# Kernel optimization log

Hardware: AMD Instinct MI355X
Metric: run time of the kernel (lower is better)

The kernel has to match this reference:

```python
import jax, jax.numpy as jnp
import numpy as np

VOL_RANGE = (-40.0, -40.0, -1.0, 40.0, 40.0, 5.4)
VOXEL = 0.8
SCENE = tuple(int((VOL_RANGE[i + 3] - VOL_RANGE[i]) / VOXEL) for i in range(3))  # (100, 100, 8)
B, G, F = 1, 128, 16


def _make_grid():
    # generate_grid(scene_shape, offset=0.5) * voxel_size + vol_range[:3]
    axes = [(jnp.arange(s, dtype=jnp.float32) + 0.5) * VOXEL + VOL_RANGE[i]
            for i, s in enumerate(SCENE)]
    gx, gy, gz = jnp.meshgrid(*axes, indexing='ij')
    return jnp.stack([gx, gy, gz], axis=-1).reshape(-1, 3)  # (N, 3)


def setup_inputs() -> dict:
    key = jax.random.key(0)
    k1, k2, k3, k4 = jax.random.split(key, 4)
    lo = jnp.array(VOL_RANGE[:3], dtype=jnp.float32)
    hi = jnp.array(VOL_RANGE[3:], dtype=jnp.float32)
    means3d = lo + jax.random.uniform(k1, (B, G, 3), dtype=jnp.float32) * (hi - lo)
    opacities = jax.random.uniform(k2, (B, G, 1), dtype=jnp.float32)
    features = jax.random.normal(k3, (B, G, F), dtype=jnp.float32)
    A = jax.random.normal(k4, (B, G, 3, 3), dtype=jnp.float32)
    covariances = jnp.einsum('bgij,bgkj->bgik', A, A) + 0.1 * jnp.eye(3, dtype=jnp.float32)
    return {
        'grid_coords': _make_grid(),
        'means3d': means3d,
        'opacities': opacities,
        'features': features,
        'covariances': covariances,
    }


def _splat_into_3d(grid_coords, means3d, opacities, covariances, features):
    # grid_coords: (N,3); means3d: (B,G,3); opacities: (B,G,1);
    # covariances: (B,G,3,3); features: (B,G,F)
    b, g, _ = means3d.shape
    n = grid_coords.shape[0]
    f = features.shape[-1]
    dtype = means3d.dtype

    def step(carry, xs):
        dens, feats, cnts = carry                 # (B,N,1), (B,N,F), (B,N,1)
        mean, opac, cov, feat = xs                # (B,3), (B,1), (B,3,3), (B,F)
        diff = grid_coords[None] - mean[:, None]  # (B,N,3)
        cov_inv = jnp.linalg.inv(cov)             # (B,3,3)
        maha = jnp.einsum('bni,bij,bnj->bn', diff, cov_inv, diff)[..., None]  # (B,N,1)
        mask = (maha <= 4.0).astype(dtype)        # (B,N,1)
        cnts = cnts + mask
        denom = jnp.maximum(cnts, 1e-6)
        w = jnp.exp(-0.5 * maha)                  # (B,N,1)
        d_g = opac[:, None] * w                   # (B,N,1)
        dens = dens + mask * (d_g - dens) / denom
        f_g = (opac * feat)[:, None] * w          # (B,N,F)
        feats = feats + mask * (f_g - feats) / denom
        return (dens, feats, cnts), None

    init = (jnp.zeros((b, n, 1), dtype),
            jnp.zeros((b, n, f), dtype),
            jnp.zeros((b, n, 1), dtype))
    xs = (jnp.swapaxes(means3d, 0, 1),
          jnp.swapaxes(opacities, 0, 1),
          jnp.swapaxes(covariances, 0, 1),
          jnp.swapaxes(features, 0, 1))
    (dens, feats, _), _ = jax.lax.scan(step, init, xs)
    return dens, feats


def reference(grid_coords, means3d, opacities, features, covariances):
    dens, feats = _splat_into_3d(grid_coords, means3d, opacities, covariances, features)
    b = dens.shape[0]
    dens = dens.reshape(b, *SCENE, 1)
    feats = feats.reshape(b, *SCENE, feats.shape[-1])
    return dens, feats
```

## Files before the change

### kernel.cpp

```cpp
#include <hip/hip_runtime.h>
#include <hip/hip_bf16.h>


#define GV_F 16
#define GV_SX 100
#define GV_SY 100
#define GV_SZ 8
#define GV_SYZ (GV_SY * GV_SZ)
#define GV_LOX (-40.0f)
#define GV_LOY (-40.0f)
#define GV_LOZ (-1.0f)
#define GV_VOX 0.8f
#define GV_GMAX 128

__global__ __launch_bounds__(256)
void GaussianVoxelizer_40467181863368_kernel(
    const float* __restrict__ means,
    const float* __restrict__ opac,
    const float* __restrict__ feats,
    const float* __restrict__ covs,
    float* __restrict__ out_dens,
    float* __restrict__ out_feat,
    int N, int G)
{
    __shared__ float s_p[GV_GMAX][10];
    __shared__ float s_f[GV_GMAX][GV_F];
    __shared__ unsigned long long s_mask[4];

    const int t = threadIdx.x;
    const int wv = t >> 6;
    const int n0 = blockIdx.x * 256;
    const int nlast = min(n0 + 255, N - 1);

    const int ix_lo = n0 / GV_SYZ;
    const int ix_hi = nlast / GV_SYZ;
    const float bx0 = ((float)ix_lo + 0.5f) * GV_VOX + GV_LOX;
    const float bx1 = ((float)ix_hi + 0.5f) * GV_VOX + GV_LOX;
    float by0, by1;
    if (ix_lo == ix_hi) {
        const int iy0b = (n0 - ix_lo * GV_SYZ) >> 3;
        const int iy1b = (nlast - ix_hi * GV_SYZ) >> 3;
        by0 = ((float)iy0b + 0.5f) * GV_VOX + GV_LOY;
        by1 = ((float)iy1b + 0.5f) * GV_VOX + GV_LOY;
    } else {
        by0 = 0.5f * GV_VOX + GV_LOY;
        by1 = ((float)(GV_SY - 1) + 0.5f) * GV_VOX + GV_LOY;
    }
    const float bz0 = 0.5f * GV_VOX + GV_LOZ;
    const float bz1 = ((float)(GV_SZ - 1) + 0.5f) * GV_VOX + GV_LOZ;

    bool flag = false;
    float mx = 0.f, my = 0.f, mz = 0.f;
    float c00 = 0.f, c01 = 0.f, c02 = 0.f, c11 = 0.f, c12 = 0.f, c22 = 0.f;
    if (t < G) {
        mx = means[t * 3 + 0];
        my = means[t * 3 + 1];
        mz = means[t * 3 + 2];
        c00 = covs[t * 9 + 0];
        c01 = covs[t * 9 + 1];
        c02 = covs[t * 9 + 2];
        c11 = covs[t * 9 + 4];
        c12 = covs[t * 9 + 5];
        c22 = covs[t * 9 + 8];
        const float rx = 2.0f * sqrtf(c00) + 1e-3f;
        const float ry = 2.0f * sqrtf(c11) + 1e-3f;
        const float rz = 2.0f * sqrtf(c22) + 1e-3f;
        flag = (mx - rx <= bx1) && (mx + rx >= bx0) &&
               (my - ry <= by1) && (my + ry >= by0) &&
               (mz - rz <= bz1) && (mz + rz >= bz0);
    }

    const unsigned long long m = __ballot(flag);
    if ((t & 63) == 0) s_mask[wv] = m;
    __syncthreads();

    if (flag) {
        int pos = 0;
        #pragma unroll
        for (int i = 0; i < 4; ++i) pos += (i < wv) ? __popcll(s_mask[i]) : 0;
        const unsigned long long lt = (t & 63) ? ((1ull << (t & 63)) - 1ull) : 0ull;
        pos += __popcll(m & lt);

        const float m00 = c11 * c22 - c12 * c12;
        const float m01 = c02 * c12 - c01 * c22;
        const float m02 = c01 * c12 - c02 * c11;
        const float det = c00 * m00 + c01 * m01 + c02 * m02;
        const float s = -0.5f / det;
        const float op = opac[t];

        s_p[pos][0] = mx;
        s_p[pos][1] = my;
        s_p[pos][2] = mz;
        s_p[pos][3] = op;
        s_p[pos][4] = m00 * s;
        s_p[pos][5] = m01 * (2.0f * s);
        s_p[pos][6] = m02 * (2.0f * s);
        s_p[pos][7] = (c00 * c22 - c02 * c02) * s;
        s_p[pos][8] = (c01 * c02 - c00 * c12) * (2.0f * s);
        s_p[pos][9] = (c00 * c11 - c01 * c01) * s;

        const float4* fr = (const float4*)(feats + (size_t)t * GV_F);
        float4* fw = (float4*)(&s_f[pos][0]);
        #pragma unroll
        for (int q = 0; q < 4; ++q) {
            float4 v = fr[q];
            v.x *= op; v.y *= op; v.z *= op; v.w *= op;
            fw[q] = v;
        }
    }
    __syncthreads();
    const int L = __popcll(s_mask[0]) + __popcll(s_mask[1]) +
                  __popcll(s_mask[2]) + __popcll(s_mask[3]);

    const int n = n0 + t;
    if (n >= N) return;

    const int ix = n / GV_SYZ;
    const int rem = n - ix * GV_SYZ;
    const int iy = rem >> 3;
    const int iz = rem & 7;
    const float cx = ((float)ix + 0.5f) * GV_VOX + GV_LOX;
    const float cy = ((float)iy + 0.5f) * GV_VOX + GV_LOY;
    const float cz = ((float)iz + 0.5f) * GV_VOX + GV_LOZ;

    float cnt = 0.0f;
    float sum_d = 0.0f;
    float sum_f[GV_F];
    #pragma unroll
    for (int j = 0; j < GV_F; ++j) sum_f[j] = 0.0f;

    for (int l = 0; l < L; ++l) {
        const float dx = cx - s_p[l][0];
        const float dy = cy - s_p[l][1];
        const float dz = cz - s_p[l][2];
        float a = s_p[l][4] * dx;
        a = fmaf(s_p[l][5], dy, a);
        a = fmaf(s_p[l][6], dz, a);
        float tt = a * dx;
        float b = s_p[l][7] * dy;
        b = fmaf(s_p[l][8], dz, b);
        tt = fmaf(b, dy, tt);
        tt = fmaf(s_p[l][9] * dz, dz, tt);
        if (tt >= -2.0f) {
            const float w = __expf(tt);
            cnt += 1.0f;
            sum_d = fmaf(s_p[l][3], w, sum_d);
            #pragma unroll
            for (int j = 0; j < GV_F; ++j) sum_f[j] = fmaf(s_f[l][j], w, sum_f[j]);
        }
    }

    const float inv_c = (cnt > 0.0f) ? (1.0f / cnt) : 0.0f;
    out_dens[n] = sum_d * inv_c;
    float4* fo = (float4*)(out_feat + (size_t)n * GV_F);
    #pragma unroll
    for (int q = 0; q < 4; ++q) {
        fo[q] = make_float4(sum_f[4 * q + 0] * inv_c,
                            sum_f[4 * q + 1] * inv_c,
                            sum_f[4 * q + 2] * inv_c,
                            sum_f[4 * q + 3] * inv_c);
    }
}

extern "C" void kernel_launch(void* const* d_in, const int* in_sizes, int n_in,
                              void* d_out, int out_size, void* d_ws, size_t ws_size,
                              hipStream_t stream) {
    const float* means = (const float*)d_in[1];
    const float* opac  = (const float*)d_in[2];
    const float* feats = (const float*)d_in[3];
    const float* covs  = (const float*)d_in[4];

    const int N = in_sizes[0] / 3;
    const int G = in_sizes[2];

    float* out_dens = (float*)d_out;
    float* out_feat = (float*)d_out + N;

    const int grid_n = (N + 255) / 256;
    GaussianVoxelizer_40467181863368_kernel<<<grid_n, 256, 0, stream>>>(
        means, opac, feats, covs, out_dens, out_feat, N, G);
}
```

Before: 65.20 us.

## Tile voxels into compact 4x8x8 blocks and vectorize shared-memory Gaussian params

Each block now covers a compact 3D tile of 4 x-slices by 8 y-rows by the full z-depth, using a 2D grid, instead of a linear run of 256 voxels. Linear runs could span an x boundary and fall back to the full y range. The tighter bounding box should let more Gaussians be culled per block. Gaussian parameters are packed into float4 shared-memory records and software-prefetched one iteration ahead to reduce LDS instruction count. Tiles at the y edge carry idle threads, since 100 is not a multiple of 8.

```diff
diff --git a/kernel.cpp b/kernel.cpp
--- a/kernel.cpp
+++ b/kernel.cpp
@@ -13,6 +13,11 @@
 #define GV_VOX 0.8f
 #define GV_GMAX 128
 
+#define GV_TX 4
+#define GV_TY 8
+#define GV_NTX (GV_SX / GV_TX)
+#define GV_NTY ((GV_SY + GV_TY - 1) / GV_TY)
+
 __global__ __launch_bounds__(256)
 void GaussianVoxelizer_40467181863368_kernel(
     const float* __restrict__ means,
@@ -23,29 +28,23 @@
     float* __restrict__ out_feat,
     int N, int G)
 {
-    __shared__ float s_p[GV_GMAX][10];
-    __shared__ float s_f[GV_GMAX][GV_F];
+    __shared__ float4 s_p[GV_GMAX][3];
+    __shared__ float4 s_f[GV_GMAX][4];
     __shared__ unsigned long long s_mask[4];
 
-    const int t = threadIdx.x;
+    const int t  = threadIdx.x;
     const int wv = t >> 6;
-    const int n0 = blockIdx.x * 256;
-    const int nlast = min(n0 + 255, N - 1);
+    const int bx = blockIdx.x;
+    const int by = blockIdx.y;
 
-    const int ix_lo = n0 / GV_SYZ;
-    const int ix_hi = nlast / GV_SYZ;
+    const int ix_lo = bx * GV_TX;
+    const int ix_hi = ix_lo + GV_TX - 1;
+    const int iy_lo = by * GV_TY;
+    const int iy_hi = min(iy_lo + GV_TY - 1, GV_SY - 1);
     const float bx0 = ((float)ix_lo + 0.5f) * GV_VOX + GV_LOX;
     const float bx1 = ((float)ix_hi + 0.5f) * GV_VOX + GV_LOX;
-    float by0, by1;
-    if (ix_lo == ix_hi) {
-        const int iy0b = (n0 - ix_lo * GV_SYZ) >> 3;
-        const int iy1b = (nlast - ix_hi * GV_SYZ) >> 3;
-        by0 = ((float)iy0b + 0.5f) * GV_VOX + GV_LOY;
-        by1 = ((float)iy1b + 0.5f) * GV_VOX + GV_LOY;
-    } else {
-        by0 = 0.5f * GV_VOX + GV_LOY;
-        by1 = ((float)(GV_SY - 1) + 0.5f) * GV_VOX + GV_LOY;
-    }
+    const float by0 = ((float)iy_lo + 0.5f) * GV_VOX + GV_LOY;
+    const float by1 = ((float)iy_hi + 0.5f) * GV_VOX + GV_LOY;
     const float bz0 = 0.5f * GV_VOX + GV_LOZ;
     const float bz1 = ((float)(GV_SZ - 1) + 0.5f) * GV_VOX + GV_LOZ;
 
@@ -88,77 +87,89 @@
         const float s = -0.5f / det;
         const float op = opac[t];
 
-        s_p[pos][0] = mx;
-        s_p[pos][1] = my;
-        s_p[pos][2] = mz;
-        s_p[pos][3] = op;
-        s_p[pos][4] = m00 * s;
-        s_p[pos][5] = m01 * (2.0f * s);
-        s_p[pos][6] = m02 * (2.0f * s);
-        s_p[pos][7] = (c00 * c22 - c02 * c02) * s;
-        s_p[pos][8] = (c01 * c02 - c00 * c12) * (2.0f * s);
-        s_p[pos][9] = (c00 * c11 - c01 * c01) * s;
+        s_p[pos][0] = make_float4(mx, my, mz, op);
+        s_p[pos][1] = make_float4(m00 * s,
+                                  m01 * (2.0f * s),
+                                  m02 * (2.0f * s),
+                                  (c00 * c22 - c02 * c02) * s);
+        s_p[pos][2] = make_float4((c01 * c02 - c00 * c12) * (2.0f * s),
+                                  (c00 * c11 - c01 * c01) * s,
+                                  0.0f, 0.0f);
 
         const float4* fr = (const float4*)(feats + (size_t)t * GV_F);
-        float4* fw = (float4*)(&s_f[pos][0]);
         #pragma unroll
         for (int q = 0; q < 4; ++q) {
             float4 v = fr[q];
             v.x *= op; v.y *= op; v.z *= op; v.w *= op;
-            fw[q] = v;
+            s_f[pos][q] = v;
         }
     }
     __syncthreads();
     const int L = __popcll(s_mask[0]) + __popcll(s_mask[1]) +
                   __popcll(s_mask[2]) + __popcll(s_mask[3]);
 
-    const int n = n0 + t;
-    if (n >= N) return;
-
-    const int ix = n / GV_SYZ;
-    const int rem = n - ix * GV_SYZ;
-    const int iy = rem >> 3;
-    const int iz = rem & 7;
+    const int lx = t >> 6;
+    const int ly = (t >> 3) & 7;
+    const int lz = t & 7;
+    const int ix = ix_lo + lx;
+    const int iy = iy_lo + ly;
     const float cx = ((float)ix + 0.5f) * GV_VOX + GV_LOX;
     const float cy = ((float)iy + 0.5f) * GV_VOX + GV_LOY;
-    const float cz = ((float)iz + 0.5f) * GV_VOX + GV_LOZ;
+    const float cz = ((float)lz + 0.5f) * GV_VOX + GV_LOZ;
 
     float cnt = 0.0f;
     float sum_d = 0.0f;
-    float sum_f[GV_F];
-    #pragma unroll
-    for (int j = 0; j < GV_F; ++j) sum_f[j] = 0.0f;
+    float4 sf0 = make_float4(0.f, 0.f, 0.f, 0.f);
+    float4 sf1 = sf0, sf2 = sf0, sf3 = sf0;
 
+    float4 pa, pb, pc;
+    if (L > 0) { pa = s_p[0][0]; pb = s_p[0][1]; pc = s_p[0][2]; }
     for (int l = 0; l < L; ++l) {
-        const float dx = cx - s_p[l][0];
-        const float dy = cy - s_p[l][1];
-        const float dz = cz - s_p[l][2];
-        float a = s_p[l][4] * dx;
-        a = fmaf(s_p[l][5], dy, a);
-        a = fmaf(s_p[l][6], dz, a);
+        const int lp = (l + 1 < L) ? (l + 1) : l;
+        const float4 na = s_p[lp][0];
+        const float4 nb = s_p[lp][1];
+        const float4 nc = s_p[lp][2];
+
+        const float dx = cx - pa.x;
+        const float dy = cy - pa.y;
+        const float dz = cz - pa.z;
+        float a = pb.x * dx;
+        a = fmaf(pb.y, dy, a);
+        a = fmaf(pb.z, dz, a);
         float tt = a * dx;
-        float b = s_p[l][7] * dy;
-        b = fmaf(s_p[l][8], dz, b);
+        float b = pb.w * dy;
+        b = fmaf(pc.x, dz, b);
         tt = fmaf(b, dy, tt);
-        tt = fmaf(s_p[l][9] * dz, dz, tt);
+        tt = fmaf(pc.y * dz, dz, tt);
         if (tt >= -2.0f) {
             const float w = __expf(tt);
             cnt += 1.0f;
-            sum_d = fmaf(s_p[l][3], w, sum_d);
-            #pragma unroll
-            for (int j = 0; j < GV_F; ++j) sum_f[j] = fmaf(s_f[l][j], w, sum_f[j]);
+            sum_d = fmaf(pa.w, w, sum_d);
+            const float4 f0 = s_f[l][0];
+            const float4 f1 = s_f[l][1];
+            const float4 f2 = s_f[l][2];
+            const float4 f3 = s_f[l][3];
+            sf0.x = fmaf(f0.x, w, sf0.x); sf0.y = fmaf(f0.y, w, sf0.y);
+            sf0.z = fmaf(f0.z, w, sf0.z); sf0.w = fmaf(f0.w, w, sf0.w);
+            sf1.x = fmaf(f1.x, w, sf1.x); sf1.y = fmaf(f1.y, w, sf1.y);
+            sf1.z = fmaf(f1.z, w, sf1.z); sf1.w = fmaf(f1.w, w, sf1.w);
+            sf2.x = fmaf(f2.x, w, sf2.x); sf2.y = fmaf(f2.y, w, sf2.y);
+            sf2.z = fmaf(f2.z, w, sf2.z); sf2.w = fmaf(f2.w, w, sf2.w);
+            sf3.x = fmaf(f3.x, w, sf3.x); sf3.y = fmaf(f3.y, w, sf3.y);
+            sf3.z = fmaf(f3.z, w, sf3.z); sf3.w = fmaf(f3.w, w, sf3.w);
         }
+        pa = na; pb = nb; pc = nc;
     }
 
-    const float inv_c = (cnt > 0.0f) ? (1.0f / cnt) : 0.0f;
-    out_dens[n] = sum_d * inv_c;
-    float4* fo = (float4*)(out_feat + (size_t)n * GV_F);
-    #pragma unroll
-    for (int q = 0; q < 4; ++q) {
-        fo[q] = make_float4(sum_f[4 * q + 0] * inv_c,
-                            sum_f[4 * q + 1] * inv_c,
-                            sum_f[4 * q + 2] * inv_c,
-                            sum_f[4 * q + 3] * inv_c);
+    if (iy < GV_SY) {
+        const int n = ix * GV_SYZ + iy * GV_SZ + lz;
+        const float inv_c = (cnt > 0.0f) ? (1.0f / cnt) : 0.0f;
+        out_dens[n] = sum_d * inv_c;
+        float4* fo = (float4*)(out_feat + (size_t)n * GV_F);
+        fo[0] = make_float4(sf0.x * inv_c, sf0.y * inv_c, sf0.z * inv_c, sf0.w * inv_c);
+        fo[1] = make_float4(sf1.x * inv_c, sf1.y * inv_c, sf1.z * inv_c, sf1.w * inv_c);
+        fo[2] = make_float4(sf2.x * inv_c, sf2.y * inv_c, sf2.z * inv_c, sf2.w * inv_c);
+        fo[3] = make_float4(sf3.x * inv_c, sf3.y * inv_c, sf3.z * inv_c, sf3.w * inv_c);
     }
 }
 
@@ -176,7 +187,7 @@
     float* out_dens = (float*)d_out;
     float* out_feat = (float*)d_out + N;
 
-    const int grid_n = (N + 255) / 256;
-    GaussianVoxelizer_40467181863368_kernel<<<grid_n, 256, 0, stream>>>(
+    dim3 grid(GV_NTX, GV_NTY, 1);
+    GaussianVoxelizer_40467181863368_kernel<<<grid, 256, 0, stream>>>(
         means, opac, feats, covs, out_dens, out_feat, N, G);
 }
```

New measurement: 64.20 us. About the same (-1.5%).
